# Performance work log

Hardware: AMD Instinct MI355X
Metric: run time of the kernel (lower is better)

The kernel has to match this reference:

```python
import jax, jax.numpy as jnp
import numpy as np

EPS = 1e-6
NEG_INF = jnp.finfo(jnp.float32).min


def setup_inputs() -> dict:
    key = jax.random.key(0)
    ks = jax.random.split(key, 12)
    N, D, H, dh, F, V, L, B = 4, 1024, 16, 64, 4096, 32000, 2048, 1
    s = 0.02
    return {
        "x_BL": jax.random.randint(ks[0], (B, L), 0, V, dtype=jnp.int32),
        "embed": jax.random.normal(ks[1], (V, D), jnp.float32) * s,
        "pos_embed": jax.random.normal(ks[2], (L, D), jnp.float32) * s,
        "wq": jax.random.normal(ks[3], (N, D, H, dh), jnp.float32) * s,
        "wk": jax.random.normal(ks[4], (N, D, H, dh), jnp.float32) * s,
        "wv": jax.random.normal(ks[5], (N, D, H, dh), jnp.float32) * s,
        "wo": jax.random.normal(ks[6], (N, H, dh, D), jnp.float32) * s,
        "gate_w": jax.random.normal(ks[7], (N, D, F), jnp.float32) * s,
        "val_w": jax.random.normal(ks[8], (N, D, F), jnp.float32) * s,
        "ffn_out_w": jax.random.normal(ks[9], (N, F, D), jnp.float32) * s,
        "ln1_s": jnp.ones((N, D), jnp.float32),
        "ln2_s": jnp.ones((N, D), jnp.float32),
        "final_ln_s": jnp.ones((D,), jnp.float32),
    }


def rmsnorm(x, scale):
    var = jnp.mean(jnp.square(x), axis=-1, keepdims=True)
    return x * jax.lax.rsqrt(var + EPS) * scale


def attention(x_BLD, wq, wk, wv, wo):
    # wq/wk/wv: [D,H,dh]; wo: [H,dh,D]
    q = jnp.einsum('bld,dhk->blhk', x_BLD, wq)
    k = jnp.einsum('bld,dhk->blhk', x_BLD, wk)
    v = jnp.einsum('bld,dhk->blhk', x_BLD, wv)
    dh = wq.shape[-1]
    a = jnp.einsum('bqhd,bkhd->bhqk', q, k) / (dh ** 0.5)
    L = x_BLD.shape[1]
    mask = jnp.tril(jnp.ones((1, 1, L, L), dtype=jnp.bool_))
    a = jnp.where(mask, a, NEG_INF)
    a = jax.nn.softmax(a, axis=-1)
    o = jnp.einsum('bhqk,bkhd->bqhd', a, v)
    return jnp.einsum('bqhd,hdD->bqD', o, wo)


def ffn(x_BLD, gate_w, val_w, out_w):
    g = jax.nn.swish(jnp.einsum('bld,df->blf', x_BLD, gate_w))
    y = jnp.einsum('bld,df->blf', x_BLD, val_w) * g
    return jnp.einsum('blf,fd->bld', y, out_w)


def reference(x_BL, embed, pos_embed, wq, wk, wv, wo, gate_w, val_w,
              ffn_out_w, ln1_s, ln2_s, final_ln_s):
    x = embed[x_BL]                              # [B,L,D]
    L = x_BL.shape[1]
    x = x + pos_embed[jnp.arange(L)][None, :, :]
    N = wq.shape[0]
    for i in range(N):
        a = attention(rmsnorm(x, ln1_s[i]), wq[i], wk[i], wv[i], wo[i])
        f = ffn(rmsnorm(x, ln2_s[i]), gate_w[i], val_w[i], ffn_out_w[i])
        x = x + a + f
    x = rmsnorm(x, final_ln_s)
    logits = jnp.einsum('bld,vd->blv', x, embed)  # tied embedding attend
    return logits
```

## Files before the change

### kernel.cpp

```cpp
#include <hip/hip_runtime.h>
#include <cstdint>
#include <cstddef>

#define L_SEQ 2048
#define DMODEL 1024
#define NHEAD 16
#define DHEAD 64
#define FFN_F 4096
#define VOCAB 32000
#define NLAYER 4

typedef __attribute__((ext_vector_type(8))) short short8;
typedef __attribute__((ext_vector_type(4))) float f32x4;

__device__ __forceinline__ unsigned short f2bf(float f) {
  unsigned int u = __float_as_uint(f);
  u += 0x7fffu + ((u >> 16) & 1u);
  return (unsigned short)(u >> 16);
}
__device__ __forceinline__ float b2f(unsigned short h) {
  return __uint_as_float(((unsigned int)h) << 16);
}
__device__ __forceinline__ float toF(float v) { return v; }
__device__ __forceinline__ float toF(unsigned short v) { return b2f(v); }

__device__ __forceinline__ void glds16(const unsigned short* g, unsigned short* l) {
  __builtin_amdgcn_global_load_lds(
      (const __attribute__((address_space(1))) unsigned int*)g,
      (__attribute__((address_space(3))) unsigned int*)l, 16, 0, 0);
}

__device__ __forceinline__ float rmax16(float v) {
  v = fmaxf(v, __shfl_xor(v, 1));
  v = fmaxf(v, __shfl_xor(v, 2));
  v = fmaxf(v, __shfl_xor(v, 4));
  v = fmaxf(v, __shfl_xor(v, 8));
  return v;
}
__device__ __forceinline__ float rsum16(float v) {
  v += __shfl_xor(v, 1);
  v += __shfl_xor(v, 2);
  v += __shfl_xor(v, 4);
  v += __shfl_xor(v, 8);
  return v;
}

#define MFMA(ACC, AF, BF) \
  ACC = __builtin_amdgcn_mfma_f32_16x16x32_bf16(AF, BF, ACC, 0, 0, 0)

enum { E_F32 = 0, E_BF16 = 1, E_SWIGLU = 2, E_PART = 3 };

template <int EPI>
__global__ __launch_bounds__(512, 2) void gemm8p(
    const unsigned short* __restrict__ A, const unsigned short* __restrict__ B,
    void* __restrict__ Cg, int M, int N, int K, int lda, int ldb, int ldc,
    float alpha, int nby)
{
  const int nwg = gridDim.x;
  const int orig = blockIdx.x;
  const int q = nwg >> 3, r = nwg & 7;
  const int xcd = orig & 7, rest = orig >> 3;
  const int wgid = (xcd < r ? xcd * (q + 1) : r * (q + 1) + (xcd - r) * q) + rest;
  const int by = wgid % nby, bx = wgid / nby;
  const int mb = by * 256, nb = bx * 256;

  __shared__ __align__(16) unsigned short As_[2][256 * 64];
  __shared__ __align__(16) unsigned short Bs_[2][256 * 64];

  const int tid = threadIdx.x;
  const int lane = tid & 63;
  const int w = tid >> 6;
  const int wm = (w >> 2) * 128;
  const int wn = (w & 3) * 64;
  const int lr = lane & 15;
  const int lg = lane >> 4;
  const int srow = lane >> 3;
  const int scol = ((lane & 7) ^ srow) * 8;
  const int slot0 = (lg ^ (lr & 7)) * 8;
  const int slot1 = ((4 + lg) ^ (lr & 7)) * 8;

  f32x4 acc[8][4];
#pragma unroll
  for (int i = 0; i < 8; i++)
#pragma unroll
    for (int j = 0; j < 4; j++) acc[i][j] = (f32x4){0.f, 0.f, 0.f, 0.f};

  const unsigned short* Ab = A + (size_t)(mb + srow) * lda + scol;
  const unsigned short* Bb = B + (size_t)(nb + srow) * ldb + scol;

  auto stageA = [&](int t, int R) {
    const int s = t & 1, kb = t << 6;
#pragma unroll
    for (int c = 0; c < 2; c++) {
      int cid = w * 2 + c;
      int rb = ((cid >> 3) << 7) + R * 64 + ((cid & 7) << 3);
      glds16(Ab + (size_t)rb * lda + kb, &As_[s][rb * 64]);
    }
  };
  auto stageB = [&](int t, int R) {
    const int s = t & 1, kb = t << 6;
#pragma unroll
    for (int c = 0; c < 2; c++) {
      int cid = w * 2 + c;
      int rb = ((cid >> 2) << 6) + R * 32 + ((cid & 3) << 3);
      glds16(Bb + (size_t)rb * ldb + kb, &Bs_[s][rb * 64]);
    }
  };

  const int nk = K >> 6;
  stageA(0, 0); stageA(0, 1); stageB(0, 0); stageB(0, 1);
  stageA(1, 0); stageB(1, 0); stageB(1, 1);
  asm volatile("s_waitcnt vmcnt(6)" ::: "memory");
  __builtin_amdgcn_s_barrier();

  short8 a[4][2], b0[2][2], b1[2][2];

  for (int t = 0; t < nk; ++t) {
    const int s = t & 1;
    const unsigned short* Asb = &As_[s][0];
    const unsigned short* Bsb = &Bs_[s][0];

#pragma unroll
    for (int i = 0; i < 4; i++) {
      a[i][0] = *(const short8*)&Asb[(wm + i * 16 + lr) * 64 + slot0];
      a[i][1] = *(const short8*)&Asb[(wm + i * 16 + lr) * 64 + slot1];
    }
#pragma unroll
    for (int j = 0; j < 2; j++) {
      b0[j][0] = *(const short8*)&Bsb[(wn + j * 16 + lr) * 64 + slot0];
      b0[j][1] = *(const short8*)&Bsb[(wn + j * 16 + lr) * 64 + slot1];
    }
    if (t + 1 < nk) stageA(t + 1, 1);
    __builtin_amdgcn_s_barrier();
    asm volatile("s_waitcnt lgkmcnt(0)" ::: "memory");
    __builtin_amdgcn_sched_barrier(0);
    __builtin_amdgcn_s_setprio(1);
#pragma unroll
    for (int kk = 0; kk < 2; kk++)
#pragma unroll
      for (int i = 0; i < 4; i++)
#pragma unroll
        for (int j = 0; j < 2; j++) MFMA(acc[i][j], a[i][kk], b0[j][kk]);
    __builtin_amdgcn_s_setprio(0);
    __builtin_amdgcn_s_barrier();

#pragma unroll
    for (int j = 0; j < 2; j++) {
      b1[j][0] = *(const short8*)&Bsb[(wn + 32 + j * 16 + lr) * 64 + slot0];
      b1[j][1] = *(const short8*)&Bsb[(wn + 32 + j * 16 + lr) * 64 + slot1];
    }
    if (t + 2 < nk) stageA(t + 2, 0);
    __builtin_amdgcn_s_barrier();
    asm volatile("s_waitcnt lgkmcnt(0)" ::: "memory");
    __builtin_amdgcn_sched_barrier(0);
    __builtin_amdgcn_s_setprio(1);
#pragma unroll
    for (int kk = 0; kk < 2; kk++)
#pragma unroll
      for (int i = 0; i < 4; i++)
#pragma unroll
        for (int j = 0; j < 2; j++) MFMA(acc[i][2 + j], a[i][kk], b1[j][kk]);
    __builtin_amdgcn_s_setprio(0);
    __builtin_amdgcn_s_barrier();

#pragma unroll
    for (int i = 0; i < 4; i++) {
      a[i][0] = *(const short8*)&Asb[(wm + 64 + i * 16 + lr) * 64 + slot0];
      a[i][1] = *(const short8*)&Asb[(wm + 64 + i * 16 + lr) * 64 + slot1];
    }
    if (t + 2 < nk) stageB(t + 2, 0);
    __builtin_amdgcn_s_barrier();
    asm volatile("s_waitcnt lgkmcnt(0)" ::: "memory");
    __builtin_amdgcn_sched_barrier(0);
    __builtin_amdgcn_s_setprio(1);
#pragma unroll
    for (int kk = 0; kk < 2; kk++)
#pragma unroll
      for (int i = 0; i < 4; i++)
#pragma unroll
        for (int j = 0; j < 2; j++) MFMA(acc[4 + i][2 + j], a[i][kk], b1[j][kk]);
    __builtin_amdgcn_s_setprio(0);
    __builtin_amdgcn_s_barrier();

    if (t + 2 < nk) stageB(t + 2, 1);
    __builtin_amdgcn_s_barrier();
    __builtin_amdgcn_sched_barrier(0);
    __builtin_amdgcn_s_setprio(1);
#pragma unroll
    for (int kk = 0; kk < 2; kk++)
#pragma unroll
      for (int i = 0; i < 4; i++)
#pragma unroll
        for (int j = 0; j < 2; j++) MFMA(acc[4 + i][j], a[i][kk], b0[j][kk]);
    __builtin_amdgcn_s_setprio(0);
    if (t + 2 < nk) {
      asm volatile("s_waitcnt vmcnt(6)" ::: "memory");
    } else {
      asm volatile("s_waitcnt vmcnt(0)" ::: "memory");
    }
    __builtin_amdgcn_s_barrier();
    __builtin_amdgcn_sched_barrier(0);
  }

#pragma unroll
  for (int i = 0; i < 8; i++) {
#pragma unroll
    for (int j = 0; j < 4; j++) {
      int oc = nb + wn + 16 * j + lr;
#pragma unroll
      for (int r4 = 0; r4 < 4; r4++) {
        int orow = mb + wm + 16 * i + lg * 4 + r4;
        float v = acc[i][j][r4] * alpha;
        if (EPI == E_F32) {
          ((float*)Cg)[(size_t)orow * ldc + oc] = v;
        } else if (EPI == E_BF16) {
          ((unsigned short*)Cg)[(size_t)orow * ldc + oc] = f2bf(v);
        } else if (EPI == E_SWIGLU) {
          float other = __shfl_xor(v, 1);
          float g = (lane & 1) ? other : v;
          float vv = (lane & 1) ? v : other;
          float sw = g / (1.0f + expf(-g)) * vv;
          if (!(lane & 1))
            ((unsigned short*)Cg)[(size_t)orow * ldc + (oc >> 1)] = f2bf(sw);
        }
      }
    }
  }
}

template <int EPI>
__global__ __launch_bounds__(256) void gemm_fast(
    const unsigned short* __restrict__ A, const unsigned short* __restrict__ B,
    void* __restrict__ Cg, int M, int N, int K, int lda, int ldb, int ldc,
    float alpha, int nbx)
{
  const int nwg = gridDim.x;
  const int orig = blockIdx.x;
  const int q = nwg >> 3, r = nwg & 7;
  const int xcd = orig & 7, rest = orig >> 3;
  const int wgid = (xcd < r ? xcd * (q + 1) : r * (q + 1) + (xcd - r) * q) + rest;
  const int bx = wgid % nbx, by = wgid / nbx;
  const int mb = by * 128;
  const int nb = bx * 128;

  const int Keff = (EPI == E_PART) ? (K >> 1) : K;
  const int koff = (EPI == E_PART) ? blockIdx.z * Keff : 0;

  __shared__ __align__(16) unsigned short As[2][128 * 64];
  __shared__ __align__(16) unsigned short Bs[2][128 * 64];

  const int tid = threadIdx.x;
  const int lane = tid & 63;
  const int wave = tid >> 6;
  const int wm = (wave >> 1) * 64;
  const int wn = (wave & 1) * 64;
  const int lr = lane & 15;
  const int lg = lane >> 4;

  const int srow = lane >> 3;
  const int scol = ((lane & 7) ^ srow) * 8;

  f32x4 acc[4][4];
#pragma unroll
  for (int i = 0; i < 4; i++)
#pragma unroll
    for (int j = 0; j < 4; j++) acc[i][j] = (f32x4){0.f, 0.f, 0.f, 0.f};

  const unsigned short* Abase = A + (size_t)(mb + wave * 32 + srow) * lda + koff + scol;
  const unsigned short* Bbase = B + (size_t)(nb + wave * 32 + srow) * ldb + koff + scol;

  auto stage = [&](int kb, int b) {
#pragma unroll
    for (int c = 0; c < 4; c++)
      glds16(Abase + (size_t)(c * 8) * lda + kb, &As[b][(wave * 32 + c * 8) * 64]);
#pragma unroll
    for (int c = 0; c < 4; c++)
      glds16(Bbase + (size_t)(c * 8) * ldb + kb, &Bs[b][(wave * 32 + c * 8) * 64]);
  };

  stage(0, 0);
  __syncthreads();
  int cur = 0;
  const int nk = Keff >> 6;

  for (int t = 0; t < nk; ++t) {
    if (t + 1 < nk) stage((t + 1) << 6, cur ^ 1);

    short8 af[2][4], bfb[2][4];
#pragma unroll
    for (int h = 0; h < 2; h++) {
      const int swz = ((h * 4 + lg) ^ (lr & 7)) * 8;
#pragma unroll
      for (int i = 0; i < 4; i++) {
        af[h][i] = *(const short8*)&As[cur][(wm + 16 * i + lr) * 64 + swz];
        bfb[h][i] = *(const short8*)&Bs[cur][(wn + 16 * i + lr) * 64 + swz];
      }
    }
#pragma unroll
    for (int h = 0; h < 2; h++)
#pragma unroll
      for (int i = 0; i < 4; i++)
#pragma unroll
        for (int j = 0; j < 4; j++) MFMA(acc[i][j], af[h][i], bfb[h][j]);

    __syncthreads();
    cur ^= 1;
  }

#pragma unroll
  for (int i = 0; i < 4; i++) {
#pragma unroll
    for (int j = 0; j < 4; j++) {
      int oc = nb + wn + 16 * j + lr;
#pragma unroll
      for (int r4 = 0; r4 < 4; r4++) {
        int orow = mb + wm + 16 * i + lg * 4 + r4;
        float v = acc[i][j][r4] * alpha;
        if (EPI == E_F32) {
          ((float*)Cg)[(size_t)orow * ldc + oc] = v;
        } else if (EPI == E_BF16) {
          ((unsigned short*)Cg)[(size_t)orow * ldc + oc] = f2bf(v);
        } else {
          float* C = (float*)Cg + (size_t)blockIdx.z * ((size_t)L_SEQ * DMODEL);
          C[(size_t)orow * ldc + oc] = v;
        }
      }
    }
  }
}

__global__ __launch_bounds__(256) void flash_attn(
    const unsigned short* __restrict__ Qg, const unsigned short* __restrict__ Kg,
    const unsigned short* __restrict__ Vt, unsigned short* __restrict__ Og,
    int ldq, int ldo)
{
  const int qb = blockIdx.x;
  const int h = blockIdx.y;
  const int tid = threadIdx.x;
  const int lane = tid & 63;
  const int w = tid >> 6;
  const int lr = lane & 15;
  const int lg = lane >> 4;

  __shared__ __align__(16) unsigned short KsL[2][64 * 64];
  __shared__ __align__(16) unsigned short VsL[2][64 * 64];
  __shared__ __align__(16) unsigned short Ps[4][32 * 64];

  const int srow = lane >> 3;
  const int scol = ((lane & 7) ^ srow) * 8;

  short8 qf[2][2];
#pragma unroll
  for (int i = 0; i < 2; i++)
#pragma unroll
    for (int kk = 0; kk < 2; kk++)
      qf[i][kk] = *(const short8*)(Qg +
          (size_t)(qb * 128 + w * 32 + i * 16 + lr) * ldq + h * 64 + kk * 32 + lg * 8);

  f32x4 acc_o[2][4];
  float m_st[2][4], l_st[2][4];
#pragma unroll
  for (int i = 0; i < 2; i++)
#pragma unroll
    for (int j = 0; j < 4; j++) acc_o[i][j] = (f32x4){0.f, 0.f, 0.f, 0.f};
#pragma unroll
  for (int i = 0; i < 2; i++)
#pragma unroll
    for (int r = 0; r < 4; r++) { m_st[i][r] = -1e30f; l_st[i][r] = 0.f; }

  const int ntiles = 2 * qb + 2;
  const int qmin = qb * 128 + w * 32;

  auto stage = [&](int t, int buf) {
#pragma unroll
    for (int c = 0; c < 2; c++) {
      glds16(Kg + (size_t)(t * 64 + w * 16 + c * 8 + srow) * ldq + h * 64 + scol,
             &KsL[buf][(w * 16 + c * 8) * 64]);
      glds16(Vt + (size_t)(h * 64 + w * 16 + c * 8 + srow) * L_SEQ + t * 64 + scol,
             &VsL[buf][(w * 16 + c * 8) * 64]);
    }
  };

  stage(0, 0);
  __syncthreads();
  int buf = 0;

  for (int t = 0; t < ntiles; t++) {
    if (t + 1 < ntiles) stage(t + 1, buf ^ 1);

    f32x4 sa[2][4];
#pragma unroll
    for (int i = 0; i < 2; i++)
#pragma unroll
      for (int j = 0; j < 4; j++) sa[i][j] = (f32x4){0.f, 0.f, 0.f, 0.f};
#pragma unroll
    for (int kk = 0; kk < 2; kk++) {
      short8 kf[4];
#pragma unroll
      for (int j = 0; j < 4; j++)
        kf[j] = *(const short8*)&KsL[buf][(j * 16 + lr) * 64 + ((kk * 4 + lg) ^ (lr & 7)) * 8];
#pragma unroll
      for (int i = 0; i < 2; i++)
#pragma unroll
        for (int j = 0; j < 4; j++) MFMA(sa[i][j], qf[i][kk], kf[j]);
    }

    const bool diag = (t * 64 + 63) > qmin;
#pragma unroll
    for (int i = 0; i < 2; i++)
#pragma unroll
      for (int j = 0; j < 4; j++)
#pragma unroll
        for (int r = 0; r < 4; r++) {
          float s = sa[i][j][r] * 0.125f;
          if (diag) {
            int kg = t * 64 + j * 16 + lr;
            int qg = qmin + i * 16 + lg * 4 + r;
            if (kg > qg) s = -1e30f;
          }
          sa[i][j][r] = s;
        }

    float fsc[2][4], mnew[2][4];
#pragma unroll
    for (int i = 0; i < 2; i++)
#pragma unroll
      for (int r = 0; r < 4; r++) {
        float mx = fmaxf(fmaxf(sa[i][0][r], sa[i][1][r]), fmaxf(sa[i][2][r], sa[i][3][r]));
        mx = rmax16(mx);
        float mn = fmaxf(m_st[i][r], mx);
        mnew[i][r] = mn;
        fsc[i][r] = __expf(m_st[i][r] - mn);
        m_st[i][r] = mn;
      }
#pragma unroll
    for (int i = 0; i < 2; i++)
#pragma unroll
      for (int r = 0; r < 4; r++) {
        float ls = 0.f;
#pragma unroll
        for (int j = 0; j < 4; j++) {
          float p = __expf(sa[i][j][r] - mnew[i][r]);
          sa[i][j][r] = p;
          ls += p;
        }
        ls = rsum16(ls);
        l_st[i][r] = l_st[i][r] * fsc[i][r] + ls;
      }
#pragma unroll
    for (int i = 0; i < 2; i++)
#pragma unroll
      for (int j = 0; j < 4; j++)
#pragma unroll
        for (int r = 0; r < 4; r++) acc_o[i][j][r] *= fsc[i][r];

#pragma unroll
    for (int i = 0; i < 2; i++)
#pragma unroll
      for (int j = 0; j < 4; j++)
#pragma unroll
        for (int r = 0; r < 4; r++) {
          int qrl = lg * 4 + r;
          int idx = (i * 16 + qrl) * 64 + (((j * 2 + (lr >> 3)) ^ (qrl & 7)) * 8) + (lr & 7);
          Ps[w][idx] = f2bf(sa[i][j][r]);
        }

#pragma unroll
    for (int kk = 0; kk < 2; kk++) {
      short8 pf[2], vf[4];
#pragma unroll
      for (int i = 0; i < 2; i++)
        pf[i] = *(const short8*)&Ps[w][(i * 16 + lr) * 64 + ((kk * 4 + lg) ^ (lr & 7)) * 8];
#pragma unroll
      for (int j = 0; j < 4; j++)
        vf[j] = *(const short8*)&VsL[buf][(j * 16 + lr) * 64 + ((kk * 4 + lg) ^ (lr & 7)) * 8];
#pragma unroll
      for (int i = 0; i < 2; i++)
#pragma unroll
        for (int j = 0; j < 4; j++) MFMA(acc_o[i][j], pf[i], vf[j]);
    }

    __syncthreads();
    buf ^= 1;
  }

  float inv[2][4];
#pragma unroll
  for (int i = 0; i < 2; i++)
#pragma unroll
    for (int r = 0; r < 4; r++) inv[i][r] = 1.0f / l_st[i][r];
#pragma unroll
  for (int i = 0; i < 2; i++)
#pragma unroll
    for (int j = 0; j < 4; j++)
#pragma unroll
      for (int r = 0; r < 4; r++) {
        size_t row = qmin + i * 16 + lg * 4 + r;
        Og[row * ldo + h * 64 + j * 16 + lr] = f2bf(acc_o[i][j][r] * inv[i][r]);
      }
}

__global__ __launch_bounds__(256) void rmsnorm_fold(
    const float* __restrict__ xin, const float* __restrict__ afp,
    const float* __restrict__ p1, const float* __restrict__ p2,
    const float* __restrict__ s1, const float* __restrict__ s2,
    unsigned short* __restrict__ o1, unsigned short* __restrict__ o2,
    float* __restrict__ xout, int fold)
{
  int row = blockIdx.x;
  int tid = threadIdx.x;
  float v[4];
  float ss = 0.f;
#pragma unroll
  for (int i = 0; i < 4; i++) {
    size_t idx = (size_t)row * DMODEL + tid + 256 * i;
    float val = xin[idx];
    if (fold) {
      val += afp[idx] + p1[idx] + p2[idx];
      xout[idx] = val;
    }
    v[i] = val;
    ss += val * val;
  }
#pragma unroll
  for (int o = 32; o > 0; o >>= 1) ss += __shfl_xor(ss, o);
  __shared__ float red[4];
  if ((tid & 63) == 0) red[tid >> 6] = ss;
  __syncthreads();
  ss = red[0] + red[1] + red[2] + red[3];
  float inv = rsqrtf(ss / DMODEL + 1e-6f);
#pragma unroll
  for (int i = 0; i < 4; i++) {
    int d = tid + 256 * i;
    size_t idx = (size_t)row * DMODEL + d;
    float nv = v[i] * inv;
    o1[idx] = f2bf(nv * s1[d]);
    if (o2) o2[idx] = f2bf(nv * s2[d]);
  }
}

template <typename Tin>
__global__ __launch_bounds__(256) void transpose_to_bf16(
    const Tin* __restrict__ in, unsigned short* __restrict__ out,
    int ld_in, int ld_out)
{
  __shared__ float tile[32][33];
  int c0 = blockIdx.x * 32;
  int r0 = blockIdx.y * 32;
  int tx = threadIdx.x;
  int ty = threadIdx.y;
#pragma unroll
  for (int j = 0; j < 32; j += 8)
    tile[ty + j][tx] = toF(in[(size_t)(r0 + ty + j) * ld_in + c0 + tx]);
  __syncthreads();
#pragma unroll
  for (int j = 0; j < 32; j += 8)
    out[(size_t)(c0 + ty + j) * ld_out + r0 + tx] = f2bf(tile[tx][ty + j]);
}

__global__ __launch_bounds__(256) void transpose_interleave2(
    const float* __restrict__ g, const float* __restrict__ v,
    unsigned short* __restrict__ out)
{
  __shared__ float tg[32][33], tv[32][33];
  int c0 = blockIdx.x * 32;
  int d0 = blockIdx.y * 32;
  int tx = threadIdx.x;
  int ty = threadIdx.y;
#pragma unroll
  for (int j = 0; j < 32; j += 8) {
    tg[ty + j][tx] = g[(size_t)(d0 + ty + j) * FFN_F + c0 + tx];
    tv[ty + j][tx] = v[(size_t)(d0 + ty + j) * FFN_F + c0 + tx];
  }
  __syncthreads();
#pragma unroll
  for (int j = 0; j < 32; j += 8) {
    out[(size_t)(2 * (c0 + ty + j)) * DMODEL + d0 + tx] = f2bf(tg[tx][ty + j]);
    out[(size_t)(2 * (c0 + ty + j) + 1) * DMODEL + d0 + tx] = f2bf(tv[tx][ty + j]);
  }
}

__global__ __launch_bounds__(256) void convert_f2b_kernel(
    const float* __restrict__ in, unsigned short* __restrict__ out, size_t n)
{
  size_t i = ((size_t)blockIdx.x * 256 + threadIdx.x) * 4;
  if (i + 3 < n) {
    float4 v = *(const float4*)(in + i);
    out[i] = f2bf(v.x);
    out[i + 1] = f2bf(v.y);
    out[i + 2] = f2bf(v.z);
    out[i + 3] = f2bf(v.w);
  }
}

__global__ __launch_bounds__(256) void embed_kernel(
    const int* __restrict__ ids, const float* __restrict__ emb,
    const float* __restrict__ pos, float* __restrict__ x)
{
  int l = blockIdx.x;
  int id = ids[l];
#pragma unroll
  for (int i = 0; i < 4; i++) {
    int d = threadIdx.x + 256 * i;
    x[(size_t)l * DMODEL + d] = emb[(size_t)id * DMODEL + d] + pos[(size_t)l * DMODEL + d];
  }
}

extern "C" void kernel_launch(void* const* d_in, const int* in_sizes, int n_in,
                              void* d_out, int out_size, void* d_ws, size_t ws_size,
                              hipStream_t stream)
{
  const int L = L_SEQ, D = DMODEL, F = FFN_F, V = VOCAB;
  const int* ids = (const int*)d_in[0];
  const float* embed = (const float*)d_in[1];
  const float* pos = (const float*)d_in[2];
  const float* wq = (const float*)d_in[3];
  const float* wk = (const float*)d_in[4];
  const float* wv = (const float*)d_in[5];
  const float* wo = (const float*)d_in[6];
  const float* gatew = (const float*)d_in[7];
  const float* valw = (const float*)d_in[8];
  const float* ffow = (const float*)d_in[9];
  const float* ln1 = (const float*)d_in[10];
  const float* ln2 = (const float*)d_in[11];
  const float* lnf = (const float*)d_in[12];

  char* ws = (char*)d_ws;
  size_t off = 0;
  auto alloc = [&](size_t bytes) -> void* {
    void* p = ws + off;
    off += (bytes + 255) & ~(size_t)255;
    return p;
  };
  float* x = (float*)alloc((size_t)L * D * 4);
  float* afp = (float*)alloc((size_t)L * D * 4);
  float* pbuf = (float*)alloc((size_t)2 * L * D * 4);
  unsigned short* xn1 = (unsigned short*)alloc((size_t)L * D * 2);
  unsigned short* xn2 = (unsigned short*)alloc((size_t)L * D * 2);
  unsigned short* qkvb = (unsigned short*)alloc((size_t)L * 3 * D * 2);
  unsigned short* vtb = (unsigned short*)alloc((size_t)L * D * 2);
  unsigned short* atb = (unsigned short*)alloc((size_t)L * D * 2);
  unsigned short* hb = (unsigned short*)alloc((size_t)L * F * 2);
  unsigned short* wqt = (unsigned short*)alloc((size_t)D * D * 2);
  unsigned short* wkt = (unsigned short*)alloc((size_t)D * D * 2);
  unsigned short* wvt = (unsigned short*)alloc((size_t)D * D * 2);
  unsigned short* wot = (unsigned short*)alloc((size_t)D * D * 2);
  unsigned short* gvt = (unsigned short*)alloc((size_t)2 * F * D * 2);
  unsigned short* fot = (unsigned short*)alloc((size_t)F * D * 2);
  unsigned short* embb = (unsigned short*)alloc((size_t)V * D * 2);

  dim3 blk(256);
  dim3 blk512(512);
  dim3 blkT(32, 8);

  auto gemmF = [&](int epi, const unsigned short* A, const unsigned short* B, void* C,
                   int M, int N, int K, int lda, int ldb, int ldc, float alpha) {
    int nbx = N / 128;
    dim3 grid(nbx * (M / 128));
    if (epi == E_F32)
      gemm_fast<E_F32><<<grid, blk, 0, stream>>>(A, B, C, M, N, K, lda, ldb, ldc, alpha, nbx);
    else
      gemm_fast<E_BF16><<<grid, blk, 0, stream>>>(A, B, C, M, N, K, lda, ldb, ldc, alpha, nbx);
  };

  auto gemm8 = [&](int epi, const unsigned short* A, const unsigned short* B, void* C,
                   int M, int N, int K, int lda, int ldb, int ldc, float alpha) {
    int nby = M / 256;
    dim3 grid(nby * (N / 256));
    if (epi == E_F32)
      gemm8p<E_F32><<<grid, blk512, 0, stream>>>(A, B, C, M, N, K, lda, ldb, ldc, alpha, nby);
    else if (epi == E_SWIGLU)
      gemm8p<E_SWIGLU><<<grid, blk512, 0, stream>>>(A, B, C, M, N, K, lda, ldb, ldc, alpha, nby);
    else
      gemm8p<E_BF16><<<grid, blk512, 0, stream>>>(A, B, C, M, N, K, lda, ldb, ldc, alpha, nby);
  };

  embed_kernel<<<L, blk, 0, stream>>>(ids, embed, pos, x);
  convert_f2b_kernel<<<(unsigned)((size_t)V * D / 1024), blk, 0, stream>>>(embed, embb, (size_t)V * D);

  for (int i = 0; i < NLAYER; i++) {
    const float* wqi = wq + (size_t)i * D * D;
    const float* wki = wk + (size_t)i * D * D;
    const float* wvi = wv + (size_t)i * D * D;
    const float* woi = wo + (size_t)i * D * D;
    const float* gi = gatew + (size_t)i * D * F;
    const float* vi = valw + (size_t)i * D * F;
    const float* fi = ffow + (size_t)i * F * D;

    transpose_to_bf16<float><<<dim3(D / 32, D / 32), blkT, 0, stream>>>(wqi, wqt, D, D);
    transpose_to_bf16<float><<<dim3(D / 32, D / 32), blkT, 0, stream>>>(wki, wkt, D, D);
    transpose_to_bf16<float><<<dim3(D / 32, D / 32), blkT, 0, stream>>>(wvi, wvt, D, D);
    transpose_to_bf16<float><<<dim3(D / 32, D / 32), blkT, 0, stream>>>(woi, wot, D, D);
    transpose_interleave2<<<dim3(F / 32, D / 32), blkT, 0, stream>>>(gi, vi, gvt);
    transpose_to_bf16<float><<<dim3(D / 32, F / 32), blkT, 0, stream>>>(fi, fot, D, F);

    rmsnorm_fold<<<L, blk, 0, stream>>>(x, afp, pbuf, pbuf + (size_t)L * D,
                                        ln1 + (size_t)i * D, ln2 + (size_t)i * D,
                                        xn1, xn2, x, i > 0 ? 1 : 0);

    gemmF(E_BF16, xn1, wqt, qkvb, L, 3 * D, D, D, D, 3 * D, 1.0f);

    transpose_to_bf16<unsigned short><<<dim3(D / 32, L / 32), blkT, 0, stream>>>(
        qkvb + 2 * D, vtb, 3 * D, L);

    flash_attn<<<dim3(16, 16), blk, 0, stream>>>(qkvb, qkvb + D, vtb, atb, 3 * D, D);

    gemmF(E_F32, atb, wot, afp, L, D, D, D, D, D, 1.0f);

    gemm8(E_SWIGLU, xn2, gvt, hb, L, 2 * F, D, D, D, F, 1.0f);

    {
      dim3 grid(128, 1, 2);
      gemm_fast<E_PART><<<grid, blk, 0, stream>>>(hb, fot, pbuf, L, D, F, F, F, D, 1.0f, 8);
    }
  }

  rmsnorm_fold<<<L, blk, 0, stream>>>(x, afp, pbuf, pbuf + (size_t)L * D,
                                      lnf, nullptr, xn1, nullptr, x, 1);
  gemm8(E_F32, xn1, embb, d_out, L, V, D, D, D, V, 1.0f);
}
```

Measured before the change: 1.268 ms.

## Fuse Wo projection into FFN-out GEMM, merge weight prep, rebalance flash attention

Concatenates the attention output and the SwiGLU hidden into one [L,5120] activation and stacks Wo^T with FFN-out^T. The Wo projection and the FFN down-projection then run as a single split-K GEMM, which removes one GEMM launch and the separate afp buffer read in rmsnorm. All per-layer weight transposes are merged into one prep_weights launch. Flash attention moves to 64-row query blocks with 128 threads, and causal work is balanced by pairing short and long query tiles in the block ordering. The GEMM inner loop also prefetches the next tile's B fragments at the end of each iteration.

```diff
diff --git a/kernel.cpp b/kernel.cpp
--- a/kernel.cpp
+++ b/kernel.cpp
@@ -21,8 +21,6 @@
 __device__ __forceinline__ float b2f(unsigned short h) {
   return __uint_as_float(((unsigned int)h) << 16);
 }
-__device__ __forceinline__ float toF(float v) { return v; }
-__device__ __forceinline__ float toF(unsigned short v) { return b2f(v); }
 
 __device__ __forceinline__ void glds16(const unsigned short* g, unsigned short* l) {
   __builtin_amdgcn_global_load_lds(
@@ -114,6 +112,11 @@
   __builtin_amdgcn_s_barrier();
 
   short8 a[4][2], b0[2][2], b1[2][2];
+#pragma unroll
+  for (int j = 0; j < 2; j++) {
+    b0[j][0] = *(const short8*)&Bs_[0][(wn + j * 16 + lr) * 64 + slot0];
+    b0[j][1] = *(const short8*)&Bs_[0][(wn + j * 16 + lr) * 64 + slot1];
+  }
 
   for (int t = 0; t < nk; ++t) {
     const int s = t & 1;
@@ -124,11 +127,6 @@
     for (int i = 0; i < 4; i++) {
       a[i][0] = *(const short8*)&Asb[(wm + i * 16 + lr) * 64 + slot0];
       a[i][1] = *(const short8*)&Asb[(wm + i * 16 + lr) * 64 + slot1];
-    }
-#pragma unroll
-    for (int j = 0; j < 2; j++) {
-      b0[j][0] = *(const short8*)&Bsb[(wn + j * 16 + lr) * 64 + slot0];
-      b0[j][1] = *(const short8*)&Bsb[(wn + j * 16 + lr) * 64 + slot1];
     }
     if (t + 1 < nk) stageA(t + 1, 1);
     __builtin_amdgcn_s_barrier();
@@ -200,6 +198,14 @@
     }
     __builtin_amdgcn_s_barrier();
     __builtin_amdgcn_sched_barrier(0);
+    if (t + 1 < nk) {
+      const unsigned short* Bn = &Bs_[s ^ 1][0];
+#pragma unroll
+      for (int j = 0; j < 2; j++) {
+        b0[j][0] = *(const short8*)&Bn[(wn + j * 16 + lr) * 64 + slot0];
+        b0[j][1] = *(const short8*)&Bn[(wn + j * 16 + lr) * 64 + slot1];
+      }
+    }
   }
 
 #pragma unroll
@@ -329,13 +335,17 @@
   }
 }
 
-__global__ __launch_bounds__(256) void flash_attn(
+__global__ __launch_bounds__(128) void flash_attn(
     const unsigned short* __restrict__ Qg, const unsigned short* __restrict__ Kg,
     const unsigned short* __restrict__ Vt, unsigned short* __restrict__ Og,
     int ldq, int ldo)
 {
-  const int qb = blockIdx.x;
-  const int h = blockIdx.y;
+  const int bid = blockIdx.x;
+  const int slot = bid & 255, ph = bid >> 8;
+  const int h = slot >> 4;
+  const int qs = slot & 15;
+  const int qb = ph ? (31 - qs) : qs;
+
   const int tid = threadIdx.x;
   const int lane = tid & 63;
   const int w = tid >> 6;
@@ -344,7 +354,7 @@
 
   __shared__ __align__(16) unsigned short KsL[2][64 * 64];
   __shared__ __align__(16) unsigned short VsL[2][64 * 64];
-  __shared__ __align__(16) unsigned short Ps[4][32 * 64];
+  __shared__ __align__(16) unsigned short Ps[2][32 * 64];
 
   const int srow = lane >> 3;
   const int scol = ((lane & 7) ^ srow) * 8;
@@ -355,7 +365,7 @@
 #pragma unroll
     for (int kk = 0; kk < 2; kk++)
       qf[i][kk] = *(const short8*)(Qg +
-          (size_t)(qb * 128 + w * 32 + i * 16 + lr) * ldq + h * 64 + kk * 32 + lg * 8);
+          (size_t)(qb * 64 + w * 32 + i * 16 + lr) * ldq + h * 64 + kk * 32 + lg * 8);
 
   f32x4 acc_o[2][4];
   float m_st[2][4], l_st[2][4];
@@ -368,16 +378,17 @@
 #pragma unroll
     for (int r = 0; r < 4; r++) { m_st[i][r] = -1e30f; l_st[i][r] = 0.f; }
 
-  const int ntiles = 2 * qb + 2;
-  const int qmin = qb * 128 + w * 32;
+  const int ntiles = qb + 1;
+  const int qmin = qb * 64 + w * 32;
 
   auto stage = [&](int t, int buf) {
 #pragma unroll
-    for (int c = 0; c < 2; c++) {
-      glds16(Kg + (size_t)(t * 64 + w * 16 + c * 8 + srow) * ldq + h * 64 + scol,
-             &KsL[buf][(w * 16 + c * 8) * 64]);
-      glds16(Vt + (size_t)(h * 64 + w * 16 + c * 8 + srow) * L_SEQ + t * 64 + scol,
-             &VsL[buf][(w * 16 + c * 8) * 64]);
+    for (int c = 0; c < 4; c++) {
+      int row = w * 32 + c * 8 + srow;
+      glds16(Kg + (size_t)(t * 64 + row) * ldq + h * 64 + scol,
+             &KsL[buf][row * 64]);
+      glds16(Vt + (size_t)(h * 64 + row) * L_SEQ + t * 64 + scol,
+             &VsL[buf][row * 64]);
     }
   };
 
@@ -501,7 +512,7 @@
 }
 
 __global__ __launch_bounds__(256) void rmsnorm_fold(
-    const float* __restrict__ xin, const float* __restrict__ afp,
+    const float* __restrict__ xin,
     const float* __restrict__ p1, const float* __restrict__ p2,
     const float* __restrict__ s1, const float* __restrict__ s2,
     unsigned short* __restrict__ o1, unsigned short* __restrict__ o2,
@@ -516,7 +527,7 @@
     size_t idx = (size_t)row * DMODEL + tid + 256 * i;
     float val = xin[idx];
     if (fold) {
-      val += afp[idx] + p1[idx] + p2[idx];
+      val += p1[idx] + p2[idx];
       xout[idx] = val;
     }
     v[i] = val;
@@ -539,9 +550,63 @@
   }
 }
 
-template <typename Tin>
-__global__ __launch_bounds__(256) void transpose_to_bf16(
-    const Tin* __restrict__ in, unsigned short* __restrict__ out,
+__global__ __launch_bounds__(256) void prep_weights(
+    const float* __restrict__ wq, const float* __restrict__ wk,
+    const float* __restrict__ wv, const float* __restrict__ wo,
+    const float* __restrict__ gw, const float* __restrict__ vw,
+    const float* __restrict__ fw,
+    unsigned short* __restrict__ qkvw, unsigned short* __restrict__ wft,
+    unsigned short* __restrict__ gvt)
+{
+  __shared__ float t0[32][33], t1[32][33];
+  int bid = blockIdx.x;
+  int tx = threadIdx.x, ty = threadIdx.y;
+  if (bid < 4096) {
+    int j = bid >> 10, tile = bid & 1023;
+    int c0 = (tile & 31) * 32, r0 = (tile >> 5) * 32;
+    const float* src = j == 0 ? wq : j == 1 ? wk : j == 2 ? wv : wo;
+#pragma unroll
+    for (int k = 0; k < 32; k += 8)
+      t0[ty + k][tx] = src[(size_t)(r0 + ty + k) * 1024 + c0 + tx];
+    __syncthreads();
+    unsigned short* dst;
+    int ldd;
+    if (j < 3) { dst = qkvw + (size_t)j * 1024 * 1024; ldd = 1024; }
+    else { dst = wft; ldd = 5120; }
+#pragma unroll
+    for (int k = 0; k < 32; k += 8)
+      dst[(size_t)(c0 + ty + k) * ldd + r0 + tx] = f2bf(t0[tx][ty + k]);
+  } else if (bid < 8192) {
+    int tile = bid - 4096;
+    int c0 = (tile & 31) * 32;
+    int r0 = (tile >> 5) * 32;
+#pragma unroll
+    for (int k = 0; k < 32; k += 8)
+      t0[ty + k][tx] = fw[(size_t)(r0 + ty + k) * 1024 + c0 + tx];
+    __syncthreads();
+#pragma unroll
+    for (int k = 0; k < 32; k += 8)
+      wft[(size_t)(c0 + ty + k) * 5120 + 1024 + r0 + tx] = f2bf(t0[tx][ty + k]);
+  } else {
+    int tile = bid - 8192;
+    int c0 = (tile & 127) * 32;
+    int d0 = (tile >> 7) * 32;
+#pragma unroll
+    for (int k = 0; k < 32; k += 8) {
+      t0[ty + k][tx] = gw[(size_t)(d0 + ty + k) * 4096 + c0 + tx];
+      t1[ty + k][tx] = vw[(size_t)(d0 + ty + k) * 4096 + c0 + tx];
+    }
+    __syncthreads();
+#pragma unroll
+    for (int k = 0; k < 32; k += 8) {
+      gvt[(size_t)(2 * (c0 + ty + k)) * 1024 + d0 + tx] = f2bf(t0[tx][ty + k]);
+      gvt[(size_t)(2 * (c0 + ty + k) + 1) * 1024 + d0 + tx] = f2bf(t1[tx][ty + k]);
+    }
+  }
+}
+
+__global__ __launch_bounds__(256) void transpose_act(
+    const unsigned short* __restrict__ in, unsigned short* __restrict__ out,
     int ld_in, int ld_out)
 {
   __shared__ float tile[32][33];
@@ -551,33 +616,11 @@
   int ty = threadIdx.y;
 #pragma unroll
   for (int j = 0; j < 32; j += 8)
-    tile[ty + j][tx] = toF(in[(size_t)(r0 + ty + j) * ld_in + c0 + tx]);
+    tile[ty + j][tx] = b2f(in[(size_t)(r0 + ty + j) * ld_in + c0 + tx]);
   __syncthreads();
 #pragma unroll
   for (int j = 0; j < 32; j += 8)
     out[(size_t)(c0 + ty + j) * ld_out + r0 + tx] = f2bf(tile[tx][ty + j]);
-}
-
-__global__ __launch_bounds__(256) void transpose_interleave2(
-    const float* __restrict__ g, const float* __restrict__ v,
-    unsigned short* __restrict__ out)
-{
-  __shared__ float tg[32][33], tv[32][33];
-  int c0 = blockIdx.x * 32;
-  int d0 = blockIdx.y * 32;
-  int tx = threadIdx.x;
-  int ty = threadIdx.y;
-#pragma unroll
-  for (int j = 0; j < 32; j += 8) {
-    tg[ty + j][tx] = g[(size_t)(d0 + ty + j) * FFN_F + c0 + tx];
-    tv[ty + j][tx] = v[(size_t)(d0 + ty + j) * FFN_F + c0 + tx];
-  }
-  __syncthreads();
-#pragma unroll
-  for (int j = 0; j < 32; j += 8) {
-    out[(size_t)(2 * (c0 + ty + j)) * DMODEL + d0 + tx] = f2bf(tg[tx][ty + j]);
-    out[(size_t)(2 * (c0 + ty + j) + 1) * DMODEL + d0 + tx] = f2bf(tv[tx][ty + j]);
-  }
 }
 
 __global__ __launch_bounds__(256) void convert_f2b_kernel(
@@ -633,89 +676,50 @@
     return p;
   };
   float* x = (float*)alloc((size_t)L * D * 4);
-  float* afp = (float*)alloc((size_t)L * D * 4);
   float* pbuf = (float*)alloc((size_t)2 * L * D * 4);
   unsigned short* xn1 = (unsigned short*)alloc((size_t)L * D * 2);
   unsigned short* xn2 = (unsigned short*)alloc((size_t)L * D * 2);
   unsigned short* qkvb = (unsigned short*)alloc((size_t)L * 3 * D * 2);
   unsigned short* vtb = (unsigned short*)alloc((size_t)L * D * 2);
-  unsigned short* atb = (unsigned short*)alloc((size_t)L * D * 2);
-  unsigned short* hb = (unsigned short*)alloc((size_t)L * F * 2);
-  unsigned short* wqt = (unsigned short*)alloc((size_t)D * D * 2);
-  unsigned short* wkt = (unsigned short*)alloc((size_t)D * D * 2);
-  unsigned short* wvt = (unsigned short*)alloc((size_t)D * D * 2);
-  unsigned short* wot = (unsigned short*)alloc((size_t)D * D * 2);
+  unsigned short* ohb = (unsigned short*)alloc((size_t)L * 5120 * 2);
+  unsigned short* qkvw = (unsigned short*)alloc((size_t)3 * D * D * 2);
+  unsigned short* wft = (unsigned short*)alloc((size_t)D * 5120 * 2);
   unsigned short* gvt = (unsigned short*)alloc((size_t)2 * F * D * 2);
-  unsigned short* fot = (unsigned short*)alloc((size_t)F * D * 2);
   unsigned short* embb = (unsigned short*)alloc((size_t)V * D * 2);
 
   dim3 blk(256);
   dim3 blk512(512);
   dim3 blkT(32, 8);
 
-  auto gemmF = [&](int epi, const unsigned short* A, const unsigned short* B, void* C,
-                   int M, int N, int K, int lda, int ldb, int ldc, float alpha) {
-    int nbx = N / 128;
-    dim3 grid(nbx * (M / 128));
-    if (epi == E_F32)
-      gemm_fast<E_F32><<<grid, blk, 0, stream>>>(A, B, C, M, N, K, lda, ldb, ldc, alpha, nbx);
-    else
-      gemm_fast<E_BF16><<<grid, blk, 0, stream>>>(A, B, C, M, N, K, lda, ldb, ldc, alpha, nbx);
-  };
-
-  auto gemm8 = [&](int epi, const unsigned short* A, const unsigned short* B, void* C,
-                   int M, int N, int K, int lda, int ldb, int ldc, float alpha) {
-    int nby = M / 256;
-    dim3 grid(nby * (N / 256));
-    if (epi == E_F32)
-      gemm8p<E_F32><<<grid, blk512, 0, stream>>>(A, B, C, M, N, K, lda, ldb, ldc, alpha, nby);
-    else if (epi == E_SWIGLU)
-      gemm8p<E_SWIGLU><<<grid, blk512, 0, stream>>>(A, B, C, M, N, K, lda, ldb, ldc, alpha, nby);
-    else
-      gemm8p<E_BF16><<<grid, blk512, 0, stream>>>(A, B, C, M, N, K, lda, ldb, ldc, alpha, nby);
-  };
-
   embed_kernel<<<L, blk, 0, stream>>>(ids, embed, pos, x);
   convert_f2b_kernel<<<(unsigned)((size_t)V * D / 1024), blk, 0, stream>>>(embed, embb, (size_t)V * D);
 
   for (int i = 0; i < NLAYER; i++) {
-    const float* wqi = wq + (size_t)i * D * D;
-    const float* wki = wk + (size_t)i * D * D;
-    const float* wvi = wv + (size_t)i * D * D;
-    const float* woi = wo + (size_t)i * D * D;
-    const float* gi = gatew + (size_t)i * D * F;
-    const float* vi = valw + (size_t)i * D * F;
-    const float* fi = ffow + (size_t)i * F * D;
-
-    transpose_to_bf16<float><<<dim3(D / 32, D / 32), blkT, 0, stream>>>(wqi, wqt, D, D);
-    transpose_to_bf16<float><<<dim3(D / 32, D / 32), blkT, 0, stream>>>(wki, wkt, D, D);
-    transpose_to_bf16<float><<<dim3(D / 32, D / 32), blkT, 0, stream>>>(wvi, wvt, D, D);
-    transpose_to_bf16<float><<<dim3(D / 32, D / 32), blkT, 0, stream>>>(woi, wot, D, D);
-    transpose_interleave2<<<dim3(F / 32, D / 32), blkT, 0, stream>>>(gi, vi, gvt);
-    transpose_to_bf16<float><<<dim3(D / 32, F / 32), blkT, 0, stream>>>(fi, fot, D, F);
-
-    rmsnorm_fold<<<L, blk, 0, stream>>>(x, afp, pbuf, pbuf + (size_t)L * D,
+    prep_weights<<<12288, blkT, 0, stream>>>(
+        wq + (size_t)i * D * D, wk + (size_t)i * D * D, wv + (size_t)i * D * D,
+        wo + (size_t)i * D * D, gatew + (size_t)i * D * F, valw + (size_t)i * D * F,
+        ffow + (size_t)i * F * D, qkvw, wft, gvt);
+
+    rmsnorm_fold<<<L, blk, 0, stream>>>(x, pbuf, pbuf + (size_t)L * D,
                                         ln1 + (size_t)i * D, ln2 + (size_t)i * D,
                                         xn1, xn2, x, i > 0 ? 1 : 0);
 
-    gemmF(E_BF16, xn1, wqt, qkvb, L, 3 * D, D, D, D, 3 * D, 1.0f);
-
-    transpose_to_bf16<unsigned short><<<dim3(D / 32, L / 32), blkT, 0, stream>>>(
-        qkvb + 2 * D, vtb, 3 * D, L);
-
-    flash_attn<<<dim3(16, 16), blk, 0, stream>>>(qkvb, qkvb + D, vtb, atb, 3 * D, D);
-
-    gemmF(E_F32, atb, wot, afp, L, D, D, D, D, D, 1.0f);
-
-    gemm8(E_SWIGLU, xn2, gvt, hb, L, 2 * F, D, D, D, F, 1.0f);
-
-    {
-      dim3 grid(128, 1, 2);
-      gemm_fast<E_PART><<<grid, blk, 0, stream>>>(hb, fot, pbuf, L, D, F, F, F, D, 1.0f, 8);
-    }
-  }
-
-  rmsnorm_fold<<<L, blk, 0, stream>>>(x, afp, pbuf, pbuf + (size_t)L * D,
+    gemm_fast<E_BF16><<<dim3(24 * 16), blk, 0, stream>>>(
+        xn1, qkvw, qkvb, L, 3 * D, D, D, D, 3 * D, 1.0f, 24);
+
+    transpose_act<<<dim3(D / 32, L / 32), blkT, 0, stream>>>(qkvb + 2 * D, vtb, 3 * D, L);
+
+    flash_attn<<<dim3(512), dim3(128), 0, stream>>>(qkvb, qkvb + D, vtb, ohb, 3 * D, 5120);
+
+    gemm8p<E_SWIGLU><<<dim3(8 * 32), blk512, 0, stream>>>(
+        xn2, gvt, ohb + 1024, L, 2 * F, D, D, D, 5120, 1.0f, 8);
+
+    gemm_fast<E_PART><<<dim3(8 * 16, 1, 2), blk, 0, stream>>>(
+        ohb, wft, pbuf, L, D, 5120, 5120, 5120, D, 1.0f, 8);
+  }
+
+  rmsnorm_fold<<<L, blk, 0, stream>>>(x, pbuf, pbuf + (size_t)L * D,
                                       lnf, nullptr, xn1, nullptr, x, 1);
-  gemm8(E_F32, xn1, embb, d_out, L, V, D, D, D, V, 1.0f);
-}
+  gemm8p<E_F32><<<dim3(8 * 125), blk512, 0, stream>>>(
+      xn1, embb, d_out, L, V, D, D, D, V, 1.0f, 8);
+}
```

After: 1.183 ms. 1.07x faster.
